# Kernel tuning notes

Hardware: AMD Instinct MI355X
Metric: run time of the kernel (lower is better)

The kernel has to match this reference:

```python
import jax, jax.numpy as jnp
import numpy as np


def setup_inputs() -> dict:
    key = jax.random.key(0)
    k1, k2 = jax.random.split(key)
    # (C, N, 2) projected circle points; only circle 0 is used
    img_render_points = jax.random.normal(k1, (2, 4096, 2), dtype=jnp.float32) * 100.0
    # (K, M, 2) skeleton slices; only the last slice is used
    ref_catheter_skeleton = jax.random.normal(k2, (2, 32768, 2), dtype=jnp.float32) * 100.0
    return {"img_render_points": img_render_points,
            "ref_catheter_skeleton": ref_catheter_skeleton}


def reference(img_render_points, ref_catheter_skeleton):
    # first projected circle -> (N, 2)
    pts = img_render_points[0].reshape(-1, 2)
    # last skeleton slice, point order flipped (flip is math-neutral for chamfer) -> (M, 2)
    ref = ref_catheter_skeleton[-1][::-1]
    # pairwise Euclidean distances (N, M) via the squared-norm expansion
    # ||a-b||^2 = ||a||^2 + ||b||^2 - 2 a.b  (avoids materializing (N, M, 2))
    sq = (jnp.sum(pts * pts, axis=1)[:, None]
          + jnp.sum(ref * ref, axis=1)[None, :]
          - 2.0 * (pts @ ref.T))
    dist = jnp.sqrt(jnp.maximum(sq, 1e-12))  # (N, M)
    chamfer = jnp.sum(jnp.min(dist, axis=1)) + jnp.sum(jnp.min(dist, axis=0))
    return chamfer
```

## Files before the change

### kernel.cpp

```cpp
#include <hip/hip_runtime.h>


typedef float v2f __attribute__((ext_vector_type(2)));

constexpr int N_PTS = 4096;
constexpr int M_REF = 32768;

__device__ __forceinline__ v2f pk_fma(v2f a, v2f b, v2f c) {
    v2f d;
    asm("v_pk_fma_f32 %0, %1, %2, %3" : "=v"(d) : "v"(a), "v"(b), "v"(c));
    return d;
}
__device__ __forceinline__ v2f pk_mul(v2f a, v2f b) {
    v2f d;
    asm("v_pk_mul_f32 %0, %1, %2" : "=v"(d) : "v"(a), "v"(b));
    return d;
}

__global__ __launch_bounds__(512) void chamfer_fused(
    const float2* __restrict__ pts, const float2* __restrict__ refs,
    float* __restrict__ partial)
{
    __shared__ float redA[128];
    __shared__ float redB[24];
    const int tid = threadIdx.x, b = blockIdx.x;
    const int lane = tid & 63, wave = tid >> 6;
    const float4* pts4  = (const float4*)pts;
    const float4* refs4 = (const float4*)refs;

    v2f pxA[16], pyA[16]; float mnA[16];
    #pragma unroll
    for (int q = 0; q < 8; ++q) {
        const float4 o = pts4[b * 8 + q];
        pxA[2*q]   = (v2f){-2.f*o.x, -2.f*o.x};
        pyA[2*q]   = (v2f){-2.f*o.y, -2.f*o.y};
        pxA[2*q+1] = (v2f){-2.f*o.z, -2.f*o.z};
        pyA[2*q+1] = (v2f){-2.f*o.w, -2.f*o.w};
    }
    v2f rxB[16], ryB[16]; float mnB[16];
    #pragma unroll
    for (int q = 0; q < 8; ++q) {
        const float4 o = refs4[b * 64 + wave * 8 + q];
        rxB[2*q]   = (v2f){-2.f*o.x, -2.f*o.x};
        ryB[2*q]   = (v2f){-2.f*o.y, -2.f*o.y};
        rxB[2*q+1] = (v2f){-2.f*o.z, -2.f*o.z};
        ryB[2*q+1] = (v2f){-2.f*o.w, -2.f*o.w};
    }
    #pragma unroll
    for (int k = 0; k < 16; ++k) { mnA[k] = 3.0e38f; mnB[k] = 3.0e38f; }

    for (int o = 0; o < 8; ++o) {
        float4 rr[4], pp[4];
        #pragma unroll
        for (int u = 0; u < 4; ++u) {
            rr[u] = refs4[tid  + 512 * (4 * o + u)];
            pp[u] = pts4 [lane +  64 * (4 * o + u)];
        }
        #pragma unroll
        for (int u = 0; u < 4; ++u) {
            const v2f rx2 = (v2f){rr[u].x, rr[u].z};
            const v2f ry2 = (v2f){rr[u].y, rr[u].w};
            const v2f rz2 = pk_fma(rx2, rx2, pk_mul(ry2, ry2));
            #pragma unroll
            for (int k = 0; k < 16; ++k) {
                const v2f d2 = pk_fma(pxA[k], rx2, pk_fma(pyA[k], ry2, rz2));
                mnA[k] = fminf(fminf(mnA[k], d2.x), d2.y);
            }
            const v2f px2 = (v2f){pp[u].x, pp[u].z};
            const v2f py2 = (v2f){pp[u].y, pp[u].w};
            const v2f pz2 = pk_fma(px2, px2, pk_mul(py2, py2));
            #pragma unroll
            for (int k = 0; k < 16; ++k) {
                const v2f d2 = pk_fma(rxB[k], px2, pk_fma(ryB[k], py2, pz2));
                mnB[k] = fminf(fminf(mnB[k], d2.x), d2.y);
            }
        }
    }

    #pragma unroll
    for (int k = 0; k < 16; ++k) {
        #pragma unroll
        for (int m = 1; m < 64; m <<= 1)
            mnA[k] = fminf(mnA[k], __shfl_xor(mnA[k], m, 64));
    }
    if (lane == 0) {
        #pragma unroll
        for (int k = 0; k < 16; ++k) redA[wave * 16 + k] = mnA[k];
    }
    #pragma unroll
    for (int k = 0; k < 16; ++k) {
        #pragma unroll
        for (int m = 1; m < 64; m <<= 1)
            mnB[k] = fminf(mnB[k], __shfl_xor(mnB[k], m, 64));
    }
    if (lane == 0) {
        float s = 0.f;
        #pragma unroll
        for (int k = 0; k < 16; ++k) {
            const float n2 = 0.25f * fmaf(rxB[k].x, rxB[k].x, ryB[k].x * ryB[k].x);
            s += sqrtf(fmaxf(mnB[k] + n2, 1e-12f));
        }
        redB[16 + wave] = s;
    }
    __syncthreads();
    if (tid < 16) {
        float m = redA[tid];
        #pragma unroll
        for (int w = 1; w < 8; ++w) m = fminf(m, redA[w * 16 + tid]);
        const float2 p = pts[b * 16 + tid];
        redB[tid] = sqrtf(fmaxf(m + fmaf(p.x, p.x, p.y * p.y), 1e-12f));
    }
    __syncthreads();
    if (tid == 0) {
        float t = 0.f;
        #pragma unroll
        for (int k = 0; k < 24; ++k) t += redB[k];
        partial[b] = t;
    }
}

__global__ __launch_bounds__(256) void chamfer_sum(
    const float* __restrict__ partial, float* __restrict__ out)
{
    __shared__ float ssum[4];
    const int tid = threadIdx.x;
    float d = partial[tid];
    #pragma unroll
    for (int off = 32; off > 0; off >>= 1) d += __shfl_down(d, off, 64);
    const int lane = tid & 63, wave = tid >> 6;
    if (lane == 0) ssum[wave] = d;
    __syncthreads();
    if (tid == 0) out[0] = ssum[0] + ssum[1] + ssum[2] + ssum[3];
}

extern "C" void kernel_launch(void* const* d_in, const int* in_sizes, int n_in,
                              void* d_out, int out_size, void* d_ws, size_t ws_size,
                              hipStream_t stream) {
    const float2* pts  = (const float2*)d_in[0];
    const float2* refs = ((const float2*)d_in[1]) + M_REF;

    float* partial = (float*)d_ws;
    float* out = (float*)d_out;

    chamfer_fused<<<256, 512, 0, stream>>>(pts, refs, partial);
    chamfer_sum  <<<1, 256, 0, stream>>>(partial, out);
}
```

Baseline: 29.51 us.

## Compute pairwise squared distances with FP16 MFMA using split-precision packed operands

Adds a pack kernel that encodes each point as hi/lo FP16 pieces of x, y and the scaled squared norm, laid out as MFMA fragments. The main kernel then gets full squared distances from 16x16x32 f16 matrix-core instructions instead of packed FP32 FMAs, with separate block groups handling the row and column minimum directions. This moves the O(NM) arithmetic onto the matrix cores. In exchange it adds an extra launch, workspace traffic and the precision risk of hi/lo FP16 splitting.

```diff
diff --git a/kernel.cpp b/kernel.cpp
--- a/kernel.cpp
+++ b/kernel.cpp
@@ -1,136 +1,209 @@
 #include <hip/hip_runtime.h>
 
 
-typedef float v2f __attribute__((ext_vector_type(2)));
+typedef _Float16 half8 __attribute__((ext_vector_type(8)));
+typedef float f32x4 __attribute__((ext_vector_type(4)));
 
 constexpr int N_PTS = 4096;
 constexpr int M_REF = 32768;
-
-__device__ __forceinline__ v2f pk_fma(v2f a, v2f b, v2f c) {
-    v2f d;
-    asm("v_pk_fma_f32 %0, %1, %2, %3" : "=v"(d) : "v"(a), "v"(b), "v"(c));
-    return d;
-}
-__device__ __forceinline__ v2f pk_mul(v2f a, v2f b) {
-    v2f d;
-    asm("v_pk_mul_f32 %0, %1, %2" : "=v"(d) : "v"(a), "v"(b));
-    return d;
-}
-
-__global__ __launch_bounds__(512) void chamfer_fused(
+constexpr int APo = 0;
+constexpr int BPo = 16384;
+constexpr int ARo = 16384 + 131072;
+constexpr int BRo = 16384 + 2 * 131072;
+constexpr int WS_U4 = BRo + 16384;
+
+__device__ __forceinline__ unsigned int pk2(float a, float b) {
+    _Float16 ha = (_Float16)a, hb = (_Float16)b;
+    unsigned short ua = *(unsigned short*)&ha, ub = *(unsigned short*)&hb;
+    return (unsigned int)ua | ((unsigned int)ub << 16);
+}
+
+__global__ __launch_bounds__(256) void pack_kernel(
     const float2* __restrict__ pts, const float2* __restrict__ refs,
-    float* __restrict__ partial)
+    uint4* __restrict__ ws4)
 {
-    __shared__ float redA[128];
-    __shared__ float redB[24];
+    const int gid = blockIdx.x * 256 + threadIdx.x;
+    float2 p; uint4 *Ad, *Bd;
+    if (gid < N_PTS) {
+        p = pts[gid];
+        Ad = ws4 + APo + (gid >> 4) * 64 + (gid & 15);
+        Bd = ws4 + BRo + (gid >> 4) * 64 + (gid & 15);
+    } else {
+        const int q = gid - N_PTS;
+        p = refs[q];
+        Ad = ws4 + ARo + (q >> 4) * 64 + (q & 15);
+        Bd = ws4 + BPo + (q >> 4) * 64 + (q & 15);
+    }
+    const float x = p.x, y = p.y;
+    const _Float16 xh = (_Float16)x; const float fxh = (float)xh, xl = x - fxh;
+    const _Float16 yh = (_Float16)y; const float fyh = (float)yh, yl = y - fyh;
+    const float n8 = fmaf(x, x, y * y) * 0.125f;
+    const _Float16 nh = (_Float16)n8; const float fnh = (float)nh, nl = n8 - fnh;
+    const uint4 z4 = make_uint4(0, 0, 0, 0);
+    Ad[0]  = make_uint4(pk2(-2.f*fxh, -2.f*fxh), pk2(-2.f*xl, -2.f*fyh),
+                        pk2(-2.f*fyh, -2.f*yl),  pk2(fnh, nl));
+    Ad[16] = make_uint4(pk2(8.f, 8.f), 0, 0, 0);
+    Ad[32] = z4; Ad[48] = z4;
+    Bd[0]  = make_uint4(pk2(fxh, xl), pk2(fxh, fyh), pk2(yl, fyh), pk2(8.f, 8.f));
+    Bd[16] = make_uint4(pk2(fnh, nl), 0, 0, 0);
+    Bd[32] = z4; Bd[48] = z4;
+}
+
+__global__ __launch_bounds__(512) void mfma_main(
+    const uint4* __restrict__ ws4, float* __restrict__ partial)
+{
+    __shared__ float red[1152];
     const int tid = threadIdx.x, b = blockIdx.x;
-    const int lane = tid & 63, wave = tid >> 6;
-    const float4* pts4  = (const float4*)pts;
-    const float4* refs4 = (const float4*)refs;
-
-    v2f pxA[16], pyA[16]; float mnA[16];
+    const int l = tid & 63, w = tid >> 6;
+    const f32x4 zc = {0.f, 0.f, 0.f, 0.f};
+
+    if (b < 256) {
+        uint4 ar = ws4[APo + b * 64 + l];
+        const half8 A = *reinterpret_cast<half8*>(&ar);
+        float a0 = 3e38f, a1 = 3e38f, a2 = 3e38f, a3 = 3e38f;
+        const uint4* Bb = ws4 + BPo + (w * 256) * 64 + l;
+        uint4 f0[8], f1[8];
+        #pragma unroll
+        for (int u = 0; u < 8; ++u) f0[u] = Bb[u * 64];
+        for (int s = 0; s < 16; ++s) {
+            #pragma unroll
+            for (int u = 0; u < 8; ++u) f1[u] = Bb[(16 * s + 8 + u) * 64];
+            #pragma unroll
+            for (int u = 0; u < 8; ++u) {
+                const half8 B = *reinterpret_cast<half8*>(&f0[u]);
+                const f32x4 D = __builtin_amdgcn_mfma_f32_16x16x32_f16(A, B, zc, 0, 0, 0);
+                a0 = fminf(a0, D[0]); a1 = fminf(a1, D[1]);
+                a2 = fminf(a2, D[2]); a3 = fminf(a3, D[3]);
+            }
+            if (s < 15) {
+                #pragma unroll
+                for (int u = 0; u < 8; ++u) f0[u] = Bb[(16 * s + 16 + u) * 64];
+            }
+            #pragma unroll
+            for (int u = 0; u < 8; ++u) {
+                const half8 B = *reinterpret_cast<half8*>(&f1[u]);
+                const f32x4 D = __builtin_amdgcn_mfma_f32_16x16x32_f16(A, B, zc, 0, 0, 0);
+                a0 = fminf(a0, D[0]); a1 = fminf(a1, D[1]);
+                a2 = fminf(a2, D[2]); a3 = fminf(a3, D[3]);
+            }
+        }
+        #pragma unroll
+        for (int m = 1; m < 16; m <<= 1) {
+            a0 = fminf(a0, __shfl_xor(a0, m, 64));
+            a1 = fminf(a1, __shfl_xor(a1, m, 64));
+            a2 = fminf(a2, __shfl_xor(a2, m, 64));
+            a3 = fminf(a3, __shfl_xor(a3, m, 64));
+        }
+        if ((l & 15) == 0) {
+            const int r0 = (l >> 4) * 4;
+            red[w * 16 + r0 + 0] = a0; red[w * 16 + r0 + 1] = a1;
+            red[w * 16 + r0 + 2] = a2; red[w * 16 + r0 + 3] = a3;
+        }
+        __syncthreads();
+        if (tid < 16) {
+            float m = red[tid];
+            #pragma unroll
+            for (int ww = 1; ww < 8; ++ww) m = fminf(m, red[ww * 16 + tid]);
+            red[1024 + tid] = sqrtf(fmaxf(m, 1e-12f));
+        }
+        __syncthreads();
+        if (tid == 0) {
+            float s = 0.f;
+            #pragma unroll
+            for (int k = 0; k < 16; ++k) s += red[1024 + k];
+            partial[b] = s;
+        }
+    } else {
+        const int rb = b - 256;
+        half8 Am[8];
+        #pragma unroll
+        for (int m = 0; m < 8; ++m) {
+            uint4 a = ws4[ARo + (rb * 8 + m) * 64 + l];
+            Am[m] = *reinterpret_cast<half8*>(&a);
+        }
+        float acc[8][4];
+        #pragma unroll
+        for (int m = 0; m < 8; ++m)
+            #pragma unroll
+            for (int r = 0; r < 4; ++r) acc[m][r] = 3e38f;
+        const uint4* Bb = ws4 + BRo + (w * 32) * 64 + l;
+        uint4 c0[4], c1[4];
+        #pragma unroll
+        for (int u = 0; u < 4; ++u) c0[u] = Bb[u * 64];
+        for (int s = 0; s < 4; ++s) {
+            #pragma unroll
+            for (int u = 0; u < 4; ++u) c1[u] = Bb[(8 * s + 4 + u) * 64];
+            #pragma unroll
+            for (int u = 0; u < 4; ++u) {
+                const half8 B = *reinterpret_cast<half8*>(&c0[u]);
+                #pragma unroll
+                for (int m = 0; m < 8; ++m) {
+                    const f32x4 D = __builtin_amdgcn_mfma_f32_16x16x32_f16(Am[m], B, zc, 0, 0, 0);
+                    acc[m][0] = fminf(acc[m][0], D[0]); acc[m][1] = fminf(acc[m][1], D[1]);
+                    acc[m][2] = fminf(acc[m][2], D[2]); acc[m][3] = fminf(acc[m][3], D[3]);
+                }
+            }
+            if (s < 3) {
+                #pragma unroll
+                for (int u = 0; u < 4; ++u) c0[u] = Bb[(8 * s + 8 + u) * 64];
+            }
+            #pragma unroll
+            for (int u = 0; u < 4; ++u) {
+                const half8 B = *reinterpret_cast<half8*>(&c1[u]);
+                #pragma unroll
+                for (int m = 0; m < 8; ++m) {
+                    const f32x4 D = __builtin_amdgcn_mfma_f32_16x16x32_f16(Am[m], B, zc, 0, 0, 0);
+                    acc[m][0] = fminf(acc[m][0], D[0]); acc[m][1] = fminf(acc[m][1], D[1]);
+                    acc[m][2] = fminf(acc[m][2], D[2]); acc[m][3] = fminf(acc[m][3], D[3]);
+                }
+            }
+        }
+        #pragma unroll
+        for (int m = 0; m < 8; ++m)
+            #pragma unroll
+            for (int r = 0; r < 4; ++r)
+                #pragma unroll
+                for (int mk = 1; mk < 16; mk <<= 1)
+                    acc[m][r] = fminf(acc[m][r], __shfl_xor(acc[m][r], mk, 64));
+        if ((l & 15) == 0) {
+            const int r0 = (l >> 4) * 4;
+            #pragma unroll
+            for (int m = 0; m < 8; ++m)
+                #pragma unroll
+                for (int r = 0; r < 4; ++r)
+                    red[w * 128 + m * 16 + r0 + r] = acc[m][r];
+        }
+        __syncthreads();
+        if (tid < 128) {
+            float mn = red[tid];
+            #pragma unroll
+            for (int ww = 1; ww < 8; ++ww) mn = fminf(mn, red[ww * 128 + tid]);
+            float d = sqrtf(fmaxf(mn, 1e-12f));
+            #pragma unroll
+            for (int off = 32; off > 0; off >>= 1) d += __shfl_down(d, off, 64);
+            if ((tid & 63) == 0) red[1024 + (tid >> 6)] = d;
+        }
+        __syncthreads();
+        if (tid == 0) partial[b] = red[1024] + red[1025];
+    }
+}
+
+__global__ __launch_bounds__(512) void sum_kernel(
+    const float* __restrict__ partial, float* __restrict__ out)
+{
+    __shared__ float ss[8];
+    const int tid = threadIdx.x;
+    float v = partial[tid];
     #pragma unroll
-    for (int q = 0; q < 8; ++q) {
-        const float4 o = pts4[b * 8 + q];
-        pxA[2*q]   = (v2f){-2.f*o.x, -2.f*o.x};
-        pyA[2*q]   = (v2f){-2.f*o.y, -2.f*o.y};
-        pxA[2*q+1] = (v2f){-2.f*o.z, -2.f*o.z};
-        pyA[2*q+1] = (v2f){-2.f*o.w, -2.f*o.w};
-    }
-    v2f rxB[16], ryB[16]; float mnB[16];
-    #pragma unroll
-    for (int q = 0; q < 8; ++q) {
-        const float4 o = refs4[b * 64 + wave * 8 + q];
-        rxB[2*q]   = (v2f){-2.f*o.x, -2.f*o.x};
-        ryB[2*q]   = (v2f){-2.f*o.y, -2.f*o.y};
-        rxB[2*q+1] = (v2f){-2.f*o.z, -2.f*o.z};
-        ryB[2*q+1] = (v2f){-2.f*o.w, -2.f*o.w};
-    }
-    #pragma unroll
-    for (int k = 0; k < 16; ++k) { mnA[k] = 3.0e38f; mnB[k] = 3.0e38f; }
-
-    for (int o = 0; o < 8; ++o) {
-        float4 rr[4], pp[4];
-        #pragma unroll
-        for (int u = 0; u < 4; ++u) {
-            rr[u] = refs4[tid  + 512 * (4 * o + u)];
-            pp[u] = pts4 [lane +  64 * (4 * o + u)];
-        }
-        #pragma unroll
-        for (int u = 0; u < 4; ++u) {
-            const v2f rx2 = (v2f){rr[u].x, rr[u].z};
-            const v2f ry2 = (v2f){rr[u].y, rr[u].w};
-            const v2f rz2 = pk_fma(rx2, rx2, pk_mul(ry2, ry2));
-            #pragma unroll
-            for (int k = 0; k < 16; ++k) {
-                const v2f d2 = pk_fma(pxA[k], rx2, pk_fma(pyA[k], ry2, rz2));
-                mnA[k] = fminf(fminf(mnA[k], d2.x), d2.y);
-            }
-            const v2f px2 = (v2f){pp[u].x, pp[u].z};
-            const v2f py2 = (v2f){pp[u].y, pp[u].w};
-            const v2f pz2 = pk_fma(px2, px2, pk_mul(py2, py2));
-            #pragma unroll
-            for (int k = 0; k < 16; ++k) {
-                const v2f d2 = pk_fma(rxB[k], px2, pk_fma(ryB[k], py2, pz2));
-                mnB[k] = fminf(fminf(mnB[k], d2.x), d2.y);
-            }
-        }
-    }
-
-    #pragma unroll
-    for (int k = 0; k < 16; ++k) {
-        #pragma unroll
-        for (int m = 1; m < 64; m <<= 1)
-            mnA[k] = fminf(mnA[k], __shfl_xor(mnA[k], m, 64));
-    }
-    if (lane == 0) {
-        #pragma unroll
-        for (int k = 0; k < 16; ++k) redA[wave * 16 + k] = mnA[k];
-    }
-    #pragma unroll
-    for (int k = 0; k < 16; ++k) {
-        #pragma unroll
-        for (int m = 1; m < 64; m <<= 1)
-            mnB[k] = fminf(mnB[k], __shfl_xor(mnB[k], m, 64));
-    }
-    if (lane == 0) {
-        float s = 0.f;
-        #pragma unroll
-        for (int k = 0; k < 16; ++k) {
-            const float n2 = 0.25f * fmaf(rxB[k].x, rxB[k].x, ryB[k].x * ryB[k].x);
-            s += sqrtf(fmaxf(mnB[k] + n2, 1e-12f));
-        }
-        redB[16 + wave] = s;
-    }
-    __syncthreads();
-    if (tid < 16) {
-        float m = redA[tid];
-        #pragma unroll
-        for (int w = 1; w < 8; ++w) m = fminf(m, redA[w * 16 + tid]);
-        const float2 p = pts[b * 16 + tid];
-        redB[tid] = sqrtf(fmaxf(m + fmaf(p.x, p.x, p.y * p.y), 1e-12f));
-    }
+    for (int off = 32; off > 0; off >>= 1) v += __shfl_down(v, off, 64);
+    if ((tid & 63) == 0) ss[tid >> 6] = v;
     __syncthreads();
     if (tid == 0) {
         float t = 0.f;
         #pragma unroll
-        for (int k = 0; k < 24; ++k) t += redB[k];
-        partial[b] = t;
+        for (int k = 0; k < 8; ++k) t += ss[k];
+        out[0] = t;
     }
-}
-
-__global__ __launch_bounds__(256) void chamfer_sum(
-    const float* __restrict__ partial, float* __restrict__ out)
-{
-    __shared__ float ssum[4];
-    const int tid = threadIdx.x;
-    float d = partial[tid];
-    #pragma unroll
-    for (int off = 32; off > 0; off >>= 1) d += __shfl_down(d, off, 64);
-    const int lane = tid & 63, wave = tid >> 6;
-    if (lane == 0) ssum[wave] = d;
-    __syncthreads();
-    if (tid == 0) out[0] = ssum[0] + ssum[1] + ssum[2] + ssum[3];
 }
 
 extern "C" void kernel_launch(void* const* d_in, const int* in_sizes, int n_in,
@@ -139,9 +212,11 @@
     const float2* pts  = (const float2*)d_in[0];
     const float2* refs = ((const float2*)d_in[1]) + M_REF;
 
-    float* partial = (float*)d_ws;
+    uint4* ws4 = (uint4*)d_ws;
+    float* partial = (float*)(ws4 + WS_U4);
     float* out = (float*)d_out;
 
-    chamfer_fused<<<256, 512, 0, stream>>>(pts, refs, partial);
-    chamfer_sum  <<<1, 256, 0, stream>>>(partial, out);
-}
+    pack_kernel<<<144, 256, 0, stream>>>(pts, refs, ws4);
+    mfma_main  <<<512, 512, 0, stream>>>(ws4, partial);
+    sum_kernel <<<1, 512, 0, stream>>>(partial, out);
+}
```

New measurement: 39.49 us. 1.34x slower.
